# Kernel optimization log

Hardware: AMD Instinct MI355X
Metric: run time of the kernel (lower is better)

Reference implementation:

```python
import jax, jax.numpy as jnp
import numpy as np

B, T, D_IN, D_H, N_H = 8, 1024, 512, 64, 8
PAD_TAIL = 128


def setup_inputs() -> dict:
    key = jax.random.key(0)
    ks = jax.random.split(key, 7)
    keys = jax.random.normal(ks[0], (B, T, D_IN), jnp.float32)
    queries = jax.random.normal(ks[1], (B, T, D_IN), jnp.float32)
    values = jax.random.normal(ks[2], (B, T, D_IN), jnp.float32)
    # truncated_normal(stddev=0.01) in the original; plain normal*0.01 is a faithful stand-in
    Wk = jax.random.normal(ks[3], (D_IN, D_H, N_H), jnp.float32) * 0.01
    Wq = jax.random.normal(ks[4], (D_IN, D_H, N_H), jnp.float32) * 0.01
    Wv = jax.random.normal(ks[5], (D_IN, D_H, N_H), jnp.float32) * 0.01
    key_seq = jax.random.randint(ks[6], (B, T), 0, 32000)
    key_seq = key_seq.at[:, -PAD_TAIL:].set(-1)  # -1 marks padding positions
    return {"keys": keys, "queries": queries, "values": values,
            "Wk": Wk, "Wq": Wq, "Wv": Wv, "key_seq": key_seq}


def reference(keys, queries, values, Wk, Wq, Wv, key_seq):
    # projections: (b, t, i) x (i, d, h) -> (b, t, d, h)
    Kh = jnp.einsum('bti,idh->btdh', keys, Wk)
    Qh = jnp.einsum('bti,idh->btdh', queries, Wq)
    Vh = jnp.einsum('bti,idh->btdh', values, Wv)

    # scores: i indexes keys, j indexes queries -> (b, Tk, Tq, h)
    scores = jnp.einsum('bidh,bjdh->bijh', Kh, Qh)

    dt = scores.dtype
    # padding mask over key positions (key_seq == -1 -> -1000)
    pad_mask = (-1000.0 * (1.0 - jnp.sign(key_seq + 1).astype(dt)))[:, :, None, None]
    # causal mask: disallow key index i > query index j (matrix_band_part(_, 0, -1) keeps i<=j)
    Tk, Tq = Kh.shape[1], Qh.shape[1]
    caus_mask = -1000.0 * jnp.tril(jnp.ones((Tk, Tq), dt), k=-1)
    mask = pad_mask + caus_mask[None, :, :, None]

    # NB: original adds mask BEFORE scaling, so the -1000 is also scaled. Keep that order.
    hidden_size = Kh.shape[2]
    scores = (scores + mask) / (hidden_size ** 0.5)

    # softmax over the key axis (axis=1)
    attn = jax.nn.softmax(scores, axis=1)

    # aggregate values: (b, i, j, h) x (b, i, d, h) -> (b, j, d, h)
    h_t = jnp.einsum('bijh,bidh->bjdh', attn, Vh)

    # tf.concat(tf.split(h_t, H, axis=-1), axis=2)[:, :, :, 0]
    # == per-head feature blocks laid out head-major along the feature axis
    b, j, d, nh = h_t.shape
    return h_t.transpose(0, 1, 3, 2).reshape(b, j, nh * d)
```

## Files before the change

kernel.cpp:

```cpp
#include <hip/hip_runtime.h>
#include <hip/hip_bf16.h>

#define B_SZ 8
#define T_SZ 1024
#define D_IN 512
#define D_H  64
#define N_H  8

typedef __hip_bfloat16 bf16;
using short8 = __attribute__((ext_vector_type(8))) short;
using short4v = __attribute__((ext_vector_type(4))) short;
using f32x4  = __attribute__((ext_vector_type(4))) float;

__device__ __forceinline__ unsigned short f2bf(float f) {
    union { __hip_bfloat16 b; unsigned short u; } c;
    c.b = __float2bfloat16(f);
    return c.u;
}

__global__ __launch_bounds__(256) void wt_kernel(
    const float* __restrict__ Wk, const float* __restrict__ Wq,
    const float* __restrict__ Wv, unsigned short* __restrict__ Wt)
{
    const int mat = blockIdx.y;
    const float* W = (mat == 0) ? Wk : (mat == 1) ? Wq : Wv;
    int idx = blockIdx.x * 256 + threadIdx.x;
    float v = W[idx];
    int k = idx >> 9, c = idx & 511;
    int h = c & 7, d = c >> 3;
    Wt[(((size_t)mat * 8 + h) * 64 + d) * 512 + k] = f2bf(v);
}

__global__ __launch_bounds__(256) void proj_kernel(
    const float* __restrict__ keys, const float* __restrict__ queries,
    const float* __restrict__ values,
    const unsigned short* __restrict__ Wt, unsigned short* __restrict__ KQVb)
{
    const int tid = threadIdx.x;
    const int m0  = blockIdx.x * 128;
    const int mh  = blockIdx.y;
    const int mat = mh >> 3, h = mh & 7;

    const float* X = (mat == 0) ? keys : (mat == 1) ? queries : values;
    const unsigned short* WT = Wt + (size_t)mh * (64 * 512);
    unsigned short* P = KQVb + (size_t)mat * ((size_t)B_SZ * N_H * T_SZ * D_H);

    __shared__ __align__(16) unsigned short Xst[128 * 72];
    __shared__ __align__(16) unsigned short Wst[64 * 72];

    const int wid = tid >> 6, lane = tid & 63;
    const int quad = lane >> 4, l15 = lane & 15;

    f32x4 acc[2][4];
    #pragma unroll
    for (int a = 0; a < 2; ++a)
        #pragma unroll
        for (int n = 0; n < 4; ++n) acc[a][n] = (f32x4){0.f, 0.f, 0.f, 0.f};

    const float4* X4 = (const float4*)X;

    for (int kc = 0; kc < 8; ++kc) {
        const int k0 = kc * 64;
        __syncthreads();
        #pragma unroll
        for (int q2 = 0; q2 < 8; ++q2) {
            int e = tid + q2 * 256;
            int r = e >> 4, c4 = e & 15;
            float4 v = X4[(size_t)(m0 + r) * (D_IN / 4) + (k0 >> 2) + c4];
            short4v s = {(short)f2bf(v.x), (short)f2bf(v.y),
                         (short)f2bf(v.z), (short)f2bf(v.w)};
            *(short4v*)&Xst[r * 72 + c4 * 4] = s;
        }
        #pragma unroll
        for (int q2 = 0; q2 < 2; ++q2) {
            int e = tid + q2 * 256;
            int d = e >> 3, ch = e & 7;
            *(short8*)&Wst[d * 72 + ch * 8] =
                *(const short8*)&WT[(size_t)d * 512 + k0 + ch * 8];
        }
        __syncthreads();
        #pragma unroll
        for (int ic = 0; ic < 2; ++ic) {
            short8 a0 = *(const short8*)&Xst[(wid*32      + l15) * 72 + ic*32 + quad*8];
            short8 a1 = *(const short8*)&Xst[(wid*32 + 16 + l15) * 72 + ic*32 + quad*8];
            #pragma unroll
            for (int nt = 0; nt < 4; ++nt) {
                short8 bf = *(const short8*)&Wst[(nt*16 + l15) * 72 + ic*32 + quad*8];
                acc[0][nt] = __builtin_amdgcn_mfma_f32_16x16x32_bf16(a0, bf, acc[0][nt], 0, 0, 0);
                acc[1][nt] = __builtin_amdgcn_mfma_f32_16x16x32_bf16(a1, bf, acc[1][nt], 0, 0, 0);
            }
        }
    }

    #pragma unroll
    for (int mt = 0; mt < 2; ++mt)
        #pragma unroll
        for (int r = 0; r < 4; ++r) {
            int m = m0 + wid * 32 + mt * 16 + quad * 4 + r;
            int bb = m >> 10, t = m & 1023;
            size_t base = (((size_t)(bb * N_H + h)) * T_SZ + t) * D_H;
            #pragma unroll
            for (int nt = 0; nt < 4; ++nt)
                P[base + nt * 16 + l15] = f2bf(acc[mt][r >= 0 ? mt : mt][0]),
                P[base + nt * 16 + l15] = f2bf(acc[mt][nt][r]);
        }
}

__global__ __launch_bounds__(256) void attn_kernel(
    const unsigned short* __restrict__ Qb, const unsigned short* __restrict__ Kb,
    const unsigned short* __restrict__ Vb,
    const int* __restrict__ key_seq, float* __restrict__ out)
{
    const int tid = threadIdx.x;
    const int j0  = (int)(gridDim.x - 1 - blockIdx.x) * 64;
    const int h   = blockIdx.y;
    const int b   = blockIdx.z;
    const int wid = tid >> 6, lane = tid & 63;
    const int quad = lane >> 4, l15 = lane & 15;

    __shared__ __align__(16) unsigned short Qst[64 * 72];
    __shared__ __align__(16) unsigned short Kst[64 * 72];
    __shared__ __align__(16) unsigned short VTst[64 * 72];
    __shared__ __align__(16) unsigned short Pst[4][64 * 20];
    __shared__ float spadf[64];

    const size_t bh = (size_t)(b * N_H + h) * T_SZ;

    #pragma unroll
    for (int q2 = 0; q2 < 2; ++q2) {
        int e = tid + q2 * 256;
        int j = e >> 3, ch = e & 7;
        *(short8*)&Qst[j * 72 + ch * 8] =
            *(const short8*)&Qb[(bh + j0 + j) * D_H + ch * 8];
    }
    __syncthreads();
    short8 qf0 = *(const short8*)&Qst[(wid * 16 + l15) * 72 +  0 + quad * 8];
    short8 qf1 = *(const short8*)&Qst[(wid * 16 + l15) * 72 + 32 + quad * 8];

    const int jg = j0 + wid * 16 + l15;

    float m = -1e30f, l = 0.f;
    f32x4 o0 = {0.f,0.f,0.f,0.f}, o1 = o0, o2 = o0, o3 = o0;

    const int ntiles = j0 / 64 + 1;
    for (int it64 = 0; it64 < ntiles; ++it64) {
        const int i0 = it64 * 64;
        __syncthreads();
        #pragma unroll
        for (int q2 = 0; q2 < 2; ++q2) {
            int e = tid + q2 * 256;
            int i = e >> 3, ch = e & 7;
            *(short8*)&Kst[i * 72 + ch * 8] =
                *(const short8*)&Kb[(bh + i0 + i) * D_H + ch * 8];
        }
        #pragma unroll
        for (int q2 = 0; q2 < 2; ++q2) {
            int e = tid + q2 * 256;
            int i = e & 63, ch = e >> 6;
            short8 v = *(const short8*)&Vb[(bh + i0 + i) * D_H + ch * 8];
            #pragma unroll
            for (int c = 0; c < 8; ++c)
                VTst[(ch * 8 + c) * 72 + i] = (unsigned short)v[c];
        }
        if (tid < 64)
            spadf[tid] = (key_seq[b * T_SZ + i0 + tid] == -1) ? -1000.f : 0.f;
        __syncthreads();

        float sv[16];
        #pragma unroll
        for (int it = 0; it < 4; ++it) {
            f32x4 s = {0.f, 0.f, 0.f, 0.f};
            short8 a0 = *(const short8*)&Kst[(it*16 + l15) * 72 +  0 + quad*8];
            s = __builtin_amdgcn_mfma_f32_16x16x32_bf16(a0, qf0, s, 0, 0, 0);
            short8 a1 = *(const short8*)&Kst[(it*16 + l15) * 72 + 32 + quad*8];
            s = __builtin_amdgcn_mfma_f32_16x16x32_bf16(a1, qf1, s, 0, 0, 0);
            #pragma unroll
            for (int r = 0; r < 4; ++r) {
                int iloc = it * 16 + quad * 4 + r;
                float v = s[r] + spadf[iloc];
                if (i0 + iloc > jg) v -= 1000.f;
                sv[it * 4 + r] = v * 0.125f;
            }
        }

        float mt = sv[0];
        #pragma unroll
        for (int k = 1; k < 16; ++k) mt = fmaxf(mt, sv[k]);
        mt = fmaxf(mt, __shfl_xor(mt, 16));
        mt = fmaxf(mt, __shfl_xor(mt, 32));
        const float mnew  = fmaxf(m, mt);
        const float alpha = __expf(m - mnew);
        float p[16], ls = 0.f;
        #pragma unroll
        for (int k = 0; k < 16; ++k) { p[k] = __expf(sv[k] - mnew); ls += p[k]; }
        ls += __shfl_xor(ls, 16);
        ls += __shfl_xor(ls, 32);
        l = l * alpha + ls;
        m = mnew;
        o0 *= alpha; o1 *= alpha; o2 *= alpha; o3 *= alpha;

        #pragma unroll
        for (int it = 0; it < 4; ++it)
            #pragma unroll
            for (int r = 0; r < 4; ++r)
                Pst[wid][(it * 16 + quad * 4 + r) * 20 + l15] =
                    f2bf(p[it * 4 + r]);

        short8 pf0, pf1;
        #pragma unroll
        for (int jj = 0; jj < 8; ++jj) {
            pf0[jj] = (short)Pst[wid][(     quad * 8 + jj) * 20 + l15];
            pf1[jj] = (short)Pst[wid][(32 + quad * 8 + jj) * 20 + l15];
        }

        short8 a;
        a = *(const short8*)&VTst[(     l15) * 72 +      quad * 8];
        o0 = __builtin_amdgcn_mfma_f32_16x16x32_bf16(a, pf0, o0, 0, 0, 0);
        a = *(const short8*)&VTst[(     l15) * 72 + 32 + quad * 8];
        o0 = __builtin_amdgcn_mfma_f32_16x16x32_bf16(a, pf1, o0, 0, 0, 0);
        a = *(const short8*)&VTst[(16 + l15) * 72 +      quad * 8];
        o1 = __builtin_amdgcn_mfma_f32_16x16x32_bf16(a, pf0, o1, 0, 0, 0);
        a = *(const short8*)&VTst[(16 + l15) * 72 + 32 + quad * 8];
        o1 = __builtin_amdgcn_mfma_f32_16x16x32_bf16(a, pf1, o1, 0, 0, 0);
        a = *(const short8*)&VTst[(32 + l15) * 72 +      quad * 8];
        o2 = __builtin_amdgcn_mfma_f32_16x16x32_bf16(a, pf0, o2, 0, 0, 0);
        a = *(const short8*)&VTst[(32 + l15) * 72 + 32 + quad * 8];
        o2 = __builtin_amdgcn_mfma_f32_16x16x32_bf16(a, pf1, o2, 0, 0, 0);
        a = *(const short8*)&VTst[(48 + l15) * 72 +      quad * 8];
        o3 = __builtin_amdgcn_mfma_f32_16x16x32_bf16(a, pf0, o3, 0, 0, 0);
        a = *(const short8*)&VTst[(48 + l15) * 72 + 32 + quad * 8];
        o3 = __builtin_amdgcn_mfma_f32_16x16x32_bf16(a, pf1, o3, 0, 0, 0);
    }

    const float inv = 1.f / l;
    float* op = out + ((size_t)b * T_SZ + jg) * (N_H * D_H) + h * D_H + quad * 4;
    #pragma unroll
    for (int r = 0; r < 4; ++r) {
        op[ 0 + r] = o0[r] * inv;
        op[16 + r] = o1[r] * inv;
        op[32 + r] = o2[r] * inv;
        op[48 + r] = o3[r] * inv;
    }
}

extern "C" void kernel_launch(void* const* d_in, const int* in_sizes, int n_in,
                              void* d_out, int out_size, void* d_ws, size_t ws_size,
                              hipStream_t stream) {
    const float* keys    = (const float*)d_in[0];
    const float* queries = (const float*)d_in[1];
    const float* values  = (const float*)d_in[2];
    const float* Wk      = (const float*)d_in[3];
    const float* Wq      = (const float*)d_in[4];
    const float* Wv      = (const float*)d_in[5];
    const int*   key_seq = (const int*)d_in[6];

    const size_t per = (size_t)B_SZ * N_H * T_SZ * D_H;
    unsigned short* KQVb = (unsigned short*)d_ws;
    unsigned short* Kb = KQVb;
    unsigned short* Qb = KQVb + per;
    unsigned short* Vb = KQVb + 2 * per;
    unsigned short* Wt = KQVb + 3 * per;

    wt_kernel<<<dim3(512 * 512 / 256, 3), 256, 0, stream>>>(Wk, Wq, Wv, Wt);
    proj_kernel<<<dim3((B_SZ * T_SZ) / 128, 3 * N_H), 256, 0, stream>>>(
        keys, queries, values, Wt, KQVb);
    attn_kernel<<<dim3(T_SZ / 64, N_H, B_SZ), 256, 0, stream>>>(
        Qb, Kb, Vb, key_seq, (float*)d_out);
}
```

Measured before the change: 181.6 us.

## Rework attention kernel with paired causal strips, double-buffered K/V tiles, and pad-tile skipping

```diff
diff --git a/kernel.cpp b/kernel.cpp
--- a/kernel.cpp
+++ b/kernel.cpp
@@ -8,9 +8,9 @@
 #define N_H  8
 
 typedef __hip_bfloat16 bf16;
-using short8 = __attribute__((ext_vector_type(8))) short;
+using short8  = __attribute__((ext_vector_type(8))) short;
 using short4v = __attribute__((ext_vector_type(4))) short;
-using f32x4  = __attribute__((ext_vector_type(4))) float;
+using f32x4   = __attribute__((ext_vector_type(4))) float;
 
 __device__ __forceinline__ unsigned short f2bf(float f) {
     union { __hip_bfloat16 b; unsigned short u; } c;
@@ -96,151 +96,184 @@
     for (int mt = 0; mt < 2; ++mt)
         #pragma unroll
         for (int r = 0; r < 4; ++r) {
-            int m = m0 + wid * 32 + mt * 16 + quad * 4 + r;
-            int bb = m >> 10, t = m & 1023;
+            int mrow = m0 + wid * 32 + mt * 16 + quad * 4 + r;
+            int bb = mrow >> 10, t = mrow & 1023;
             size_t base = (((size_t)(bb * N_H + h)) * T_SZ + t) * D_H;
             #pragma unroll
             for (int nt = 0; nt < 4; ++nt)
-                P[base + nt * 16 + l15] = f2bf(acc[mt][r >= 0 ? mt : mt][0]),
                 P[base + nt * 16 + l15] = f2bf(acc[mt][nt][r]);
         }
 }
 
-__global__ __launch_bounds__(256) void attn_kernel(
+#define SCALE  0.18033688f
+#define MASKV -180.33688f
+
+__global__ __launch_bounds__(512, 4) void attn_kernel(
     const unsigned short* __restrict__ Qb, const unsigned short* __restrict__ Kb,
     const unsigned short* __restrict__ Vb,
     const int* __restrict__ key_seq, float* __restrict__ out)
 {
-    const int tid = threadIdx.x;
-    const int j0  = (int)(gridDim.x - 1 - blockIdx.x) * 64;
-    const int h   = blockIdx.y;
-    const int b   = blockIdx.z;
-    const int wid = tid >> 6, lane = tid & 63;
+    const int tid  = threadIdx.x;
+    const int bid  = blockIdx.x;
+    const int pair = bid >> 6;
+    const int b    = (bid >> 3) & 7;
+    const int h    = bid & 7;
+    const int wid  = tid >> 6, lane = tid & 63;
     const int quad = lane >> 4, l15 = lane & 15;
 
-    __shared__ __align__(16) unsigned short Qst[64 * 72];
-    __shared__ __align__(16) unsigned short Kst[64 * 72];
-    __shared__ __align__(16) unsigned short VTst[64 * 72];
-    __shared__ __align__(16) unsigned short Pst[4][64 * 20];
-    __shared__ float spadf[64];
+    __shared__ __align__(16) unsigned short Kst[2][64 * 72];
+    __shared__ __align__(16) unsigned short VTst[2][64 * 72];
+    __shared__ __align__(16) float spadf[2][64];
+    __shared__ int tflags[16];
 
     const size_t bh = (size_t)(b * N_H + h) * T_SZ;
 
+    const int strip_j0 = (wid < 4) ? (15 - pair) * 64 : pair * 64;
+    const int j0w = strip_j0 + (wid & 3) * 16;
+    const int jg  = j0w + l15;
+    const int ntmax = 16 - pair;
+
+    short8 qf0 = *(const short8*)&Qb[(bh + jg) * D_H + quad * 8];
+    short8 qf1 = *(const short8*)&Qb[(bh + jg) * D_H + 32 + quad * 8];
+
+    {
+        int ka  = key_seq[b * T_SZ + wid * 64 + lane];
+        int kb2 = key_seq[b * T_SZ + 512 + wid * 64 + lane];
+        unsigned long long ba  = __ballot(ka  != -1);
+        unsigned long long bb2 = __ballot(kb2 != -1);
+        if (lane == 0) {
+            tflags[wid]     = (ba  != 0ull ? 1 : 0) | (ba  != ~0ull ? 2 : 0);
+            tflags[8 + wid] = (bb2 != 0ull ? 1 : 0) | (bb2 != ~0ull ? 2 : 0);
+        }
+    }
+
+    const int sk_row = tid >> 3, sk_c = tid & 7;
+    const int sv_i = lane, sv_ch = wid;
+    const int sv_col = (sv_i & 3) | ((sv_i & 16) >> 2) | ((sv_i & 4) << 1)
+                     | ((sv_i & 8) << 1) | (sv_i & 32);
+
+    short8 kreg = *(const short8*)&Kb[(bh + sk_row) * D_H + sk_c * 8];
+    short8 vreg = *(const short8*)&Vb[(bh + sv_i) * D_H + sv_ch * 8];
+    int ksv = (tid < 64) ? key_seq[b * T_SZ + tid] : -1;
+
+    __syncthreads();
+
+    unsigned tmask = 1u, pmask = 0u;
     #pragma unroll
-    for (int q2 = 0; q2 < 2; ++q2) {
-        int e = tid + q2 * 256;
-        int j = e >> 3, ch = e & 7;
-        *(short8*)&Qst[j * 72 + ch * 8] =
-            *(const short8*)&Qb[(bh + j0 + j) * D_H + ch * 8];
+    for (int t = 0; t < 16; ++t) {
+        int f = tflags[t];
+        tmask |= (unsigned)(f & 1) << t;
+        pmask |= (unsigned)((f >> 1) & 1) << t;
     }
+    tmask &= (unsigned)((1ull << ntmax) - 1ull);
+    tmask |= 1u;
+
+    *(short8*)&Kst[0][sk_row * 72 + sk_c * 8] = kreg;
+    #pragma unroll
+    for (int e = 0; e < 8; ++e)
+        VTst[0][(sv_ch * 8 + e) * 72 + sv_col] = (unsigned short)vreg[e];
+    if (tid < 64) spadf[0][tid] = (ksv == -1) ? MASKV : 0.f;
     __syncthreads();
-    short8 qf0 = *(const short8*)&Qst[(wid * 16 + l15) * 72 +  0 + quad * 8];
-    short8 qf1 = *(const short8*)&Qst[(wid * 16 + l15) * 72 + 32 + quad * 8];
-
-    const int jg = j0 + wid * 16 + l15;
 
     float m = -1e30f, l = 0.f;
     f32x4 o0 = {0.f,0.f,0.f,0.f}, o1 = o0, o2 = o0, o3 = o0;
 
-    const int ntiles = j0 / 64 + 1;
-    for (int it64 = 0; it64 < ntiles; ++it64) {
-        const int i0 = it64 * 64;
+    unsigned rem = tmask & ~1u;
+    int tcur = 0, nb = 0;
+    for (;;) {
+        int tnext = -1;
+        if (rem) { tnext = __ffs((int)rem) - 1; rem &= rem - 1; }
+        if (tnext >= 0) {
+            const size_t r0 = bh + tnext * 64;
+            kreg = *(const short8*)&Kb[(r0 + sk_row) * D_H + sk_c * 8];
+            vreg = *(const short8*)&Vb[(r0 + sv_i) * D_H + sv_ch * 8];
+            if (tid < 64) ksv = key_seq[b * T_SZ + tnext * 64 + tid];
+        }
+
+        const int i0 = tcur * 64;
+        if (i0 <= j0w + 15) {
+            const bool haspad = (pmask >> tcur) & 1u;
+            const bool needC  = (i0 + 63 > j0w);
+            float sv[16];
+            #pragma unroll
+            for (int it = 0; it < 4; ++it) {
+                f32x4 s = {0.f,0.f,0.f,0.f};
+                short8 a0 = *(const short8*)&Kst[nb][(it*16 + l15) * 72 + quad*8];
+                s = __builtin_amdgcn_mfma_f32_16x16x32_bf16(a0, qf0, s, 0, 0, 0);
+                short8 a1 = *(const short8*)&Kst[nb][(it*16 + l15) * 72 + 32 + quad*8];
+                s = __builtin_amdgcn_mfma_f32_16x16x32_bf16(a1, qf1, s, 0, 0, 0);
+                f32x4 sp = {0.f,0.f,0.f,0.f};
+                if (haspad) sp = *(const f32x4*)&spadf[nb][it*16 + quad*4];
+                #pragma unroll
+                for (int r = 0; r < 4; ++r) {
+                    float v = __builtin_fmaf(s[r], SCALE, sp[r]);
+                    if (needC && (i0 + it*16 + quad*4 + r > jg)) v += MASKV;
+                    sv[it*4 + r] = v;
+                }
+            }
+
+            float mt = sv[0];
+            #pragma unroll
+            for (int k = 1; k < 16; ++k) mt = fmaxf(mt, sv[k]);
+            mt = fmaxf(mt, __shfl_xor(mt, 16));
+            mt = fmaxf(mt, __shfl_xor(mt, 32));
+            const float mnew  = fmaxf(m, mt);
+            const float alpha = exp2f(m - mnew);
+            float p[16], ls = 0.f;
+            #pragma unroll
+            for (int k = 0; k < 16; ++k) {
+                p[k] = exp2f(sv[k] - mnew);
+                ls += p[k];
+            }
+            ls += __shfl_xor(ls, 16);
+            ls += __shfl_xor(ls, 32);
+            l = l * alpha + ls;
+            m = mnew;
+            o0 *= alpha; o1 *= alpha; o2 *= alpha; o3 *= alpha;
+
+            short8 pf0, pf1;
+            #pragma unroll
+            for (int e = 0; e < 8; ++e) {
+                pf0[e] = (short)f2bf(p[e]);
+                pf1[e] = (short)f2bf(p[8 + e]);
+            }
+            short8 a;
+            a = *(const short8*)&VTst[nb][(     l15) * 72 +      quad * 8];
+            o0 = __builtin_amdgcn_mfma_f32_16x16x32_bf16(a, pf0, o0, 0, 0, 0);
+            a = *(const short8*)&VTst[nb][(     l15) * 72 + 32 + quad * 8];
+            o0 = __builtin_amdgcn_mfma_f32_16x16x32_bf16(a, pf1, o0, 0, 0, 0);
+            a = *(const short8*)&VTst[nb][(16 + l15) * 72 +      quad * 8];
+            o1 = __builtin_amdgcn_mfma_f32_16x16x32_bf16(a, pf0, o1, 0, 0, 0);
+            a = *(const short8*)&VTst[nb][(16 + l15) * 72 + 32 + quad * 8];
+            o1 = __builtin_amdgcn_mfma_f32_16x16x32_bf16(a, pf1, o1, 0, 0, 0);
+            a = *(const short8*)&VTst[nb][(32 + l15) * 72 +      quad * 8];
+            o2 = __builtin_amdgcn_mfma_f32_16x16x32_bf16(a, pf0, o2, 0, 0, 0);
+            a = *(const short8*)&VTst[nb][(32 + l15) * 72 + 32 + quad * 8];
+            o2 = __builtin_amdgcn_mfma_f32_16x16x32_bf16(a, pf1, o2, 0, 0, 0);
+            a = *(const short8*)&VTst[nb][(48 + l15) * 72 +      quad * 8];
+            o3 = __builtin_amdgcn_mfma_f32_16x16x32_bf16(a, pf0, o3, 0, 0, 0);
+            a = *(const short8*)&VTst[nb][(48 + l15) * 72 + 32 + quad * 8];
+            o3 = __builtin_amdgcn_mfma_f32_16x16x32_bf16(a, pf1, o3, 0, 0, 0);
+        }
+
+        if (tnext < 0) break;
+
+        const int nb2 = nb ^ 1;
+        *(short8*)&Kst[nb2][sk_row * 72 + sk_c * 8] = kreg;
+        #pragma unroll
+        for (int e = 0; e < 8; ++e)
+            VTst[nb2][(sv_ch * 8 + e) * 72 + sv_col] = (unsigned short)vreg[e];
+        if (tid < 64) spadf[nb2][tid] = (ksv == -1) ? MASKV : 0.f;
         __syncthreads();
-        #pragma unroll
-        for (int q2 = 0; q2 < 2; ++q2) {
-            int e = tid + q2 * 256;
-            int i = e >> 3, ch = e & 7;
-            *(short8*)&Kst[i * 72 + ch * 8] =
-                *(const short8*)&Kb[(bh + i0 + i) * D_H + ch * 8];
-        }
-        #pragma unroll
-        for (int q2 = 0; q2 < 2; ++q2) {
-            int e = tid + q2 * 256;
-            int i = e & 63, ch = e >> 6;
-            short8 v = *(const short8*)&Vb[(bh + i0 + i) * D_H + ch * 8];
-            #pragma unroll
-            for (int c = 0; c < 8; ++c)
-                VTst[(ch * 8 + c) * 72 + i] = (unsigned short)v[c];
-        }
-        if (tid < 64)
-            spadf[tid] = (key_seq[b * T_SZ + i0 + tid] == -1) ? -1000.f : 0.f;
-        __syncthreads();
-
-        float sv[16];
-        #pragma unroll
-        for (int it = 0; it < 4; ++it) {
-            f32x4 s = {0.f, 0.f, 0.f, 0.f};
-            short8 a0 = *(const short8*)&Kst[(it*16 + l15) * 72 +  0 + quad*8];
-            s = __builtin_amdgcn_mfma_f32_16x16x32_bf16(a0, qf0, s, 0, 0, 0);
-            short8 a1 = *(const short8*)&Kst[(it*16 + l15) * 72 + 32 + quad*8];
-            s = __builtin_amdgcn_mfma_f32_16x16x32_bf16(a1, qf1, s, 0, 0, 0);
-            #pragma unroll
-            for (int r = 0; r < 4; ++r) {
-                int iloc = it * 16 + quad * 4 + r;
-                float v = s[r] + spadf[iloc];
-                if (i0 + iloc > jg) v -= 1000.f;
-                sv[it * 4 + r] = v * 0.125f;
-            }
-        }
-
-        float mt = sv[0];
-        #pragma unroll
-        for (int k = 1; k < 16; ++k) mt = fmaxf(mt, sv[k]);
-        mt = fmaxf(mt, __shfl_xor(mt, 16));
-        mt = fmaxf(mt, __shfl_xor(mt, 32));
-        const float mnew  = fmaxf(m, mt);
-        const float alpha = __expf(m - mnew);
-        float p[16], ls = 0.f;
-        #pragma unroll
-        for (int k = 0; k < 16; ++k) { p[k] = __expf(sv[k] - mnew); ls += p[k]; }
-        ls += __shfl_xor(ls, 16);
-        ls += __shfl_xor(ls, 32);
-        l = l * alpha + ls;
-        m = mnew;
-        o0 *= alpha; o1 *= alpha; o2 *= alpha; o3 *= alpha;
-
-        #pragma unroll
-        for (int it = 0; it < 4; ++it)
-            #pragma unroll
-            for (int r = 0; r < 4; ++r)
-                Pst[wid][(it * 16 + quad * 4 + r) * 20 + l15] =
-                    f2bf(p[it * 4 + r]);
-
-        short8 pf0, pf1;
-        #pragma unroll
-        for (int jj = 0; jj < 8; ++jj) {
-            pf0[jj] = (short)Pst[wid][(     quad * 8 + jj) * 20 + l15];
-            pf1[jj] = (short)Pst[wid][(32 + quad * 8 + jj) * 20 + l15];
-        }
-
-        short8 a;
-        a = *(const short8*)&VTst[(     l15) * 72 +      quad * 8];
-        o0 = __builtin_amdgcn_mfma_f32_16x16x32_bf16(a, pf0, o0, 0, 0, 0);
-        a = *(const short8*)&VTst[(     l15) * 72 + 32 + quad * 8];
-        o0 = __builtin_amdgcn_mfma_f32_16x16x32_bf16(a, pf1, o0, 0, 0, 0);
-        a = *(const short8*)&VTst[(16 + l15) * 72 +      quad * 8];
-        o1 = __builtin_amdgcn_mfma_f32_16x16x32_bf16(a, pf0, o1, 0, 0, 0);
-        a = *(const short8*)&VTst[(16 + l15) * 72 + 32 + quad * 8];
-        o1 = __builtin_amdgcn_mfma_f32_16x16x32_bf16(a, pf1, o1, 0, 0, 0);
-        a = *(const short8*)&VTst[(32 + l15) * 72 +      quad * 8];
-        o2 = __builtin_amdgcn_mfma_f32_16x16x32_bf16(a, pf0, o2, 0, 0, 0);
-        a = *(const short8*)&VTst[(32 + l15) * 72 + 32 + quad * 8];
-        o2 = __builtin_amdgcn_mfma_f32_16x16x32_bf16(a, pf1, o2, 0, 0, 0);
-        a = *(const short8*)&VTst[(48 + l15) * 72 +      quad * 8];
-        o3 = __builtin_amdgcn_mfma_f32_16x16x32_bf16(a, pf0, o3, 0, 0, 0);
-        a = *(const short8*)&VTst[(48 + l15) * 72 + 32 + quad * 8];
-        o3 = __builtin_amdgcn_mfma_f32_16x16x32_bf16(a, pf1, o3, 0, 0, 0);
+        tcur = tnext; nb = nb2;
     }
 
     const float inv = 1.f / l;
     float* op = out + ((size_t)b * T_SZ + jg) * (N_H * D_H) + h * D_H + quad * 4;
-    #pragma unroll
-    for (int r = 0; r < 4; ++r) {
-        op[ 0 + r] = o0[r] * inv;
-        op[16 + r] = o1[r] * inv;
-        op[32 + r] = o2[r] * inv;
-        op[48 + r] = o3[r] * inv;
-    }
+    *(f32x4*)(op +  0) = o0 * inv;
+    *(f32x4*)(op + 16) = o1 * inv;
+    *(f32x4*)(op + 32) = o2 * inv;
+    *(f32x4*)(op + 48) = o3 * inv;
 }
 
 extern "C" void kernel_launch(void* const* d_in, const int* in_sizes, int n_in,
@@ -264,6 +297,6 @@
     wt_kernel<<<dim3(512 * 512 / 256, 3), 256, 0, stream>>>(Wk, Wq, Wv, Wt);
     proj_kernel<<<dim3((B_SZ * T_SZ) / 128, 3 * N_H), 256, 0, stream>>>(
         keys, queries, values, Wt, KQVb);
-    attn_kernel<<<dim3(T_SZ / 64, N_H, B_SZ), 256, 0, stream>>>(
+    attn_kernel<<<dim3(512), dim3(512), 0, stream>>>(
         Qb, Kb, Vb, key_seq, (float*)d_out);
 }
```

New measurement: 156.8 us. 13.6% less time.
